# Performance work log

Hardware: AMD Instinct MI355X
Metric: run time of the kernel (lower is better)

## Reference

```python
import jax, jax.numpy as jnp
from jax import lax
import numpy as np

HEADS = 3
DIM_HEAD = 64
INNER = HEADS * DIM_HEAD  # 192
SCALE = DIM_HEAD ** -0.5
BN_EPS = 1e-5


def _sep_conv(x, dw, gamma, beta, mean, var, pw, stride):
    """Depthwise conv (SAME) -> BatchNorm (inference) -> 1x1 pointwise conv."""
    C = x.shape[-1]
    x = lax.conv_general_dilated(
        x, dw, window_strides=(stride, stride), padding='SAME',
        dimension_numbers=('NHWC', 'HWIO', 'NHWC'), feature_group_count=C)
    x = (x - mean) * lax.rsqrt(var + BN_EPS) * gamma + beta
    return jnp.einsum('bhwc,cd->bhwd', x, pw)


def setup_inputs() -> dict:
    key = jax.random.key(0)
    ks = jax.random.split(key, 8)
    B, H, W, C = 8, 56, 56, 192
    return {
        'x': jax.random.normal(ks[0], (B, H, W, C), dtype=jnp.float32),
        'dw_q': jax.random.normal(ks[1], (3, 3, 1, C), dtype=jnp.float32) * 0.1,
        'q_gamma': jnp.ones((C,), jnp.float32),
        'q_beta': jnp.zeros((C,), jnp.float32),
        'q_mean': jnp.zeros((C,), jnp.float32),
        'q_var': jnp.ones((C,), jnp.float32),
        'pw_q': jax.random.normal(ks[2], (C, INNER), dtype=jnp.float32) / np.sqrt(C).astype(np.float32),
        'dw_kv': jax.random.normal(ks[3], (3, 3, 1, C), dtype=jnp.float32) * 0.1,
        'kv_gamma': jnp.ones((C,), jnp.float32),
        'kv_beta': jnp.zeros((C,), jnp.float32),
        'kv_mean': jnp.zeros((C,), jnp.float32),
        'kv_var': jnp.ones((C,), jnp.float32),
        'pw_kv': jax.random.normal(ks[4], (C, 2 * INNER), dtype=jnp.float32) / np.sqrt(C).astype(np.float32),
        'out_w': jax.random.normal(ks[5], (INNER, C), dtype=jnp.float32) / np.sqrt(INNER).astype(np.float32),
        'out_b': jnp.zeros((C,), jnp.float32),
    }


def reference(x, dw_q, q_gamma, q_beta, q_mean, q_var, pw_q,
              dw_kv, kv_gamma, kv_beta, kv_mean, kv_var, pw_kv,
              out_w, out_b):
    B, H, W, C = x.shape
    q = _sep_conv(x, dw_q, q_gamma, q_beta, q_mean, q_var, pw_q, 1)      # [B,H,W,INNER]
    kv = _sep_conv(x, dw_kv, kv_gamma, kv_beta, kv_mean, kv_var, pw_kv, 2)  # [B,H/2,W/2,2*INNER]
    k, v = jnp.split(kv, 2, axis=-1)

    def split_heads(t):
        b, h, w, _ = t.shape
        return t.reshape(b, h * w, HEADS, DIM_HEAD)

    q, k, v = split_heads(q), split_heads(k), split_heads(v)  # [B,N,h,d]
    scores = jnp.einsum('bihd,bjhd->bhij', q, k) * SCALE       # [B,h,Nq,Nkv]
    attn = jax.nn.softmax(scores, axis=-1)
    o = jnp.einsum('bhij,bjhd->bihd', attn, v)                 # [B,Nq,h,d]
    o = o.reshape(B, H, W, INNER)
    return jnp.einsum('bhwc,cd->bhwd', o, out_w) + out_b
```

## Files before the change

### kernel.cpp

```cpp
#include <hip/hip_runtime.h>

namespace {
constexpr int Bb = 8, Hh = 56, Ww = 56, Cc = 192;
constexpr int NQ  = Hh * Ww;
constexpr int NKV = 28 * 28;
constexpr float EPS = 1e-5f;
}

typedef __attribute__((ext_vector_type(8))) short          bf16x8;
typedef __attribute__((ext_vector_type(4))) float          f32x4;
typedef __attribute__((ext_vector_type(8))) unsigned short u16x8;

__device__ inline unsigned short f2b(float f) {
  unsigned u = __builtin_bit_cast(unsigned, f);
  u += 0x7FFFu + ((u >> 16) & 1u);
  return (unsigned short)(u >> 16);
}

__device__ inline uint2 pack4(float a, float b, float c, float d) {
  uint2 r;
  r.x = (unsigned)f2b(a) | ((unsigned)f2b(b) << 16);
  r.y = (unsigned)f2b(c) | ((unsigned)f2b(d) << 16);
  return r;
}

__global__ __launch_bounds__(256) void prep_w_kernel(
    const float* __restrict__ pwq, const float* __restrict__ pwkv,
    const float* __restrict__ outw,
    unsigned short* __restrict__ wq, unsigned short* __restrict__ wkv,
    unsigned short* __restrict__ wo)
{
  int i = blockIdx.x * 256 + threadIdx.x;
  if (i < 36864) {
    int n = i / 192, k = i - n * 192;
    wq[i] = f2b(pwq[k * 192 + n]);
  } else if (i < 110592) {
    int j = i - 36864;
    int n = j / 192, k = j - n * 192;
    wkv[j] = f2b(pwkv[k * 384 + n]);
  } else if (i < 147456) {
    int j = i - 110592;
    int n = j / 192, k = j - n * 192;
    wo[j] = f2b(outw[k * 192 + n]);
  }
}

__global__ __launch_bounds__(256) void dwbn_bf16_kernel(
    const float* __restrict__ x, const float* __restrict__ w,
    const float* __restrict__ gamma, const float* __restrict__ beta,
    const float* __restrict__ mean, const float* __restrict__ var,
    unsigned short* __restrict__ out, int OH, int OW, int stride, int pad)
{
  int idx = blockIdx.x * 256 + threadIdx.x;
  int total = Bb * OH * OW * 48;
  if (idx >= total) return;
  int c4 = idx % 48;
  int t = idx / 48;
  int ow = t % OW; t /= OW;
  int oh = t % OH; int b = t / OH;
  const int c = c4 * 4;

  float4 acc = make_float4(0.f, 0.f, 0.f, 0.f);
#pragma unroll
  for (int kh = 0; kh < 3; ++kh) {
    int ih = oh * stride - pad + kh;
    if (ih < 0 || ih >= Hh) continue;
#pragma unroll
    for (int kw = 0; kw < 3; ++kw) {
      int iw = ow * stride - pad + kw;
      if (iw < 0 || iw >= Ww) continue;
      float4 xv = *(const float4*)&x[((size_t)(b * Hh + ih) * Ww + iw) * Cc + c];
      float4 wv = *(const float4*)&w[(kh * 3 + kw) * Cc + c];
      acc.x += xv.x * wv.x; acc.y += xv.y * wv.y;
      acc.z += xv.z * wv.z; acc.w += xv.w * wv.w;
    }
  }
  float4 gm = *(const float4*)&gamma[c];
  float4 bt = *(const float4*)&beta[c];
  float4 mn = *(const float4*)&mean[c];
  float4 vr = *(const float4*)&var[c];
  float r0 = (acc.x - mn.x) * gm.x / sqrtf(vr.x + EPS) + bt.x;
  float r1 = (acc.y - mn.y) * gm.y / sqrtf(vr.y + EPS) + bt.y;
  float r2 = (acc.z - mn.z) * gm.z / sqrtf(vr.z + EPS) + bt.z;
  float r3 = (acc.w - mn.w) * gm.w / sqrtf(vr.w + EPS) + bt.w;
  const size_t row = (size_t)(b * OH + oh) * OW + ow;
  *reinterpret_cast<uint2*>(&out[row * 192 + c]) = pack4(r0, r1, r2, r3);
}

template <int MODE>
__global__ __launch_bounds__(256) void gemm_mfma(
    const unsigned short* __restrict__ A, const unsigned short* __restrict__ Bt,
    const float* __restrict__ bias, unsigned short* __restrict__ QK,
    unsigned short* __restrict__ Vt, float* __restrict__ O32,
    int N, int NR)
{
  __shared__ unsigned short As[128][72];
  __shared__ unsigned short Bs[64][72];

  const int nbl = N >> 6;
  const int bm = blockIdx.x / nbl, bn = blockIdx.x % nbl;
  const int row0 = bm << 7, col0 = bn << 6;
  const int tid = threadIdx.x;
  const int lane = tid & 63, w = tid >> 6;
  const int lr = lane & 15, lg = lane >> 4;
  const int wm = w >> 1, wn = w & 1;

  f32x4 acc[4][2];
#pragma unroll
  for (int mr = 0; mr < 4; ++mr)
#pragma unroll
    for (int nr = 0; nr < 2; ++nr) acc[mr][nr] = (f32x4){0.f, 0.f, 0.f, 0.f};

  for (int k0 = 0; k0 < 192; k0 += 64) {
    {
      const int r = tid >> 1, c0 = (tid & 1) * 32;
      const unsigned short* src = A + (size_t)(row0 + r) * 192 + k0 + c0;
#pragma unroll
      for (int u = 0; u < 4; ++u)
        *(u16x8*)&As[r][c0 + u * 8] = *(const u16x8*)&src[u * 8];
    }
    {
      const int n = tid >> 2, c0 = (tid & 3) * 16;
      const unsigned short* src = Bt + (size_t)(col0 + n) * 192 + k0 + c0;
#pragma unroll
      for (int u = 0; u < 2; ++u)
        *(u16x8*)&Bs[n][c0 + u * 8] = *(const u16x8*)&src[u * 8];
    }
    __syncthreads();
#pragma unroll
    for (int ks = 0; ks < 2; ++ks) {
      bf16x8 a[4], b[2];
#pragma unroll
      for (int mr = 0; mr < 4; ++mr)
        a[mr] = *(const bf16x8*)&As[wm * 64 + mr * 16 + lr][ks * 32 + lg * 8];
#pragma unroll
      for (int nr = 0; nr < 2; ++nr)
        b[nr] = *(const bf16x8*)&Bs[wn * 32 + nr * 16 + lr][ks * 32 + lg * 8];
#pragma unroll
      for (int mr = 0; mr < 4; ++mr)
#pragma unroll
        for (int nr = 0; nr < 2; ++nr)
          acc[mr][nr] = __builtin_amdgcn_mfma_f32_16x16x32_bf16(a[mr], b[nr], acc[mr][nr], 0, 0, 0);
    }
    __syncthreads();
  }

#pragma unroll
  for (int mr = 0; mr < 4; ++mr) {
#pragma unroll
    for (int nr = 0; nr < 2; ++nr) {
      const int c = col0 + wn * 32 + nr * 16 + lr;
      const int rbase = row0 + wm * 64 + mr * 16 + lg * 4;
      if (MODE == 2) {
        const float bb = bias[c];
#pragma unroll
        for (int j = 0; j < 4; ++j)
          O32[(size_t)(rbase + j) * 192 + c] = acc[mr][nr][j] + bb;
      } else if (MODE == 0 || (MODE == 1 && c < 192)) {
        const int h = c >> 6, d = c & 63;
        const int b = rbase / NR;
        const int n0 = rbase - b * NR;
        const float sc = (MODE == 0) ? 0.125f : 1.0f;
#pragma unroll
        for (int j = 0; j < 4; ++j)
          QK[(((size_t)b * 3 + h) * NR + n0 + j) * 64 + d] = f2b(acc[mr][nr][j] * sc);
      } else {
        const int h = (c - 192) >> 6, d = (c - 192) & 63;
        const int b = rbase / 784;
        const int n0 = rbase - b * 784;
        uint2 v = pack4(acc[mr][nr][0], acc[mr][nr][1], acc[mr][nr][2], acc[mr][nr][3]);
        *reinterpret_cast<uint2*>(&Vt[(((size_t)b * 3 + h) * 64 + d) * 784 + n0]) = v;
      }
    }
  }
}

__global__ __launch_bounds__(256) void attn_mfma_kernel(
    const unsigned short* __restrict__ Qb, const unsigned short* __restrict__ Kb,
    const unsigned short* __restrict__ Vtb, unsigned short* __restrict__ Ob)
{
  __shared__ unsigned short Ks[64][72];
  __shared__ unsigned short Vts[64][72];
  __shared__ unsigned short Ps[64][66];
  __shared__ float ls[4][16];

  const int blk = blockIdx.x;
  const int qt = blk % 49;
  const int bh = blk / 49;
  const int n0 = qt * 64;
  const int tid = threadIdx.x;
  const int lane = tid & 63;
  const int w = tid >> 6;
  const int lr = lane & 15, lg = lane >> 4;
  const int row = tid >> 2, cc = tid & 3;

  const unsigned short* qrow = Qb + ((size_t)bh * NQ + n0 + w * 16 + lr) * 64;
  const bf16x8 aq0 = *(const bf16x8*)&qrow[lg * 8];
  const bf16x8 aq1 = *(const bf16x8*)&qrow[32 + lg * 8];

  const unsigned short* kbase = Kb + (size_t)bh * NKV * 64;
  const unsigned short* vrow  = Vtb + ((size_t)bh * 64 + row) * NKV;

  f32x4 oacc[4];
#pragma unroll
  for (int db = 0; db < 4; ++db) oacc[db] = (f32x4){0.f, 0.f, 0.f, 0.f};
  float lsum = 0.f;

  for (int kt = 0; kt < 13; ++kt) {
    __syncthreads();
    {
      const int kvg = (kt * 64 + row < NKV) ? kt * 64 + row : NKV - 1;
      const unsigned short* kp = kbase + (size_t)kvg * 64;
      *(u16x8*)&Ks[row][cc * 8]      = *(const u16x8*)&kp[cc * 8];
      *(u16x8*)&Ks[row][cc * 8 + 32] = *(const u16x8*)&kp[cc * 8 + 32];
#pragma unroll
      for (int u = 0; u < 2; ++u) {
        const int c8 = cc + 4 * u;
        const int kv0 = kt * 64 + c8 * 8;
        u16x8 vv = {0, 0, 0, 0, 0, 0, 0, 0};
        if (kv0 < NKV) vv = *(const u16x8*)&vrow[kv0];
        *(u16x8*)&Vts[row][c8 * 8] = vv;
      }
    }
    __syncthreads();

    f32x4 st[4];
#pragma unroll
    for (int nb = 0; nb < 4; ++nb) {
      const bf16x8 bk0 = *(const bf16x8*)&Ks[nb * 16 + lr][lg * 8];
      const bf16x8 bk1 = *(const bf16x8*)&Ks[nb * 16 + lr][32 + lg * 8];
      f32x4 a = (f32x4){0.f, 0.f, 0.f, 0.f};
      a = __builtin_amdgcn_mfma_f32_16x16x32_bf16(bk0, aq0, a, 0, 0, 0);
      a = __builtin_amdgcn_mfma_f32_16x16x32_bf16(bk1, aq1, a, 0, 0, 0);
      st[nb] = a;
    }

    const int kvb = kt * 64 + lg * 4;
#pragma unroll
    for (int nb = 0; nb < 4; ++nb) {
      float p[4];
#pragma unroll
      for (int r = 0; r < 4; ++r)
        p[r] = (kvb + nb * 16 + r < NKV) ? __expf(st[nb][r]) : 0.f;
      lsum += (p[0] + p[1]) + (p[2] + p[3]);
      uint2 u = pack4(p[0], p[1], p[2], p[3]);
      *reinterpret_cast<uint2*>(&Ps[w * 16 + lr][nb * 16 + lg * 4]) = u;
    }

    const bf16x8 pa0 = *(const bf16x8*)&Ps[w * 16 + lr][lg * 8];
    const bf16x8 pa1 = *(const bf16x8*)&Ps[w * 16 + lr][32 + lg * 8];
#pragma unroll
    for (int db = 0; db < 4; ++db) {
      const bf16x8 vb0 = *(const bf16x8*)&Vts[db * 16 + lr][lg * 8];
      const bf16x8 vb1 = *(const bf16x8*)&Vts[db * 16 + lr][32 + lg * 8];
      oacc[db] = __builtin_amdgcn_mfma_f32_16x16x32_bf16(pa0, vb0, oacc[db], 0, 0, 0);
      oacc[db] = __builtin_amdgcn_mfma_f32_16x16x32_bf16(pa1, vb1, oacc[db], 0, 0, 0);
    }
  }

  float l = lsum;
  l += __shfl_xor(l, 16);
  l += __shfl_xor(l, 32);
  if (lg == 0) ls[w][lr] = l;
  const float4 lv = *(const float4*)&ls[w][lg * 4];

  const int b = bh / 3, h = bh - b * 3;
  float linv[4];
#pragma unroll
  for (int j = 0; j < 4; ++j) linv[j] = 1.f / ((&lv.x)[j]);
#pragma unroll
  for (int j = 0; j < 4; ++j) {
    const int qg = n0 + w * 16 + lg * 4 + j;
    unsigned short* orow = Ob + ((size_t)b * NQ + qg) * 192 + h * 64 + lr;
#pragma unroll
    for (int db = 0; db < 4; ++db) orow[db * 16] = f2b(oacc[db][j] * linv[j]);
  }
}

extern "C" void kernel_launch(void* const* d_in, const int* in_sizes, int n_in,
                              void* d_out, int out_size, void* d_ws, size_t ws_size,
                              hipStream_t stream)
{
  const float* x        = (const float*)d_in[0];
  const float* dw_q     = (const float*)d_in[1];
  const float* q_gamma  = (const float*)d_in[2];
  const float* q_beta   = (const float*)d_in[3];
  const float* q_mean   = (const float*)d_in[4];
  const float* q_var    = (const float*)d_in[5];
  const float* pw_q     = (const float*)d_in[6];
  const float* dw_kv    = (const float*)d_in[7];
  const float* kv_gamma = (const float*)d_in[8];
  const float* kv_beta  = (const float*)d_in[9];
  const float* kv_mean  = (const float*)d_in[10];
  const float* kv_var   = (const float*)d_in[11];
  const float* pw_kv    = (const float*)d_in[12];
  const float* out_w    = (const float*)d_in[13];
  const float* out_b    = (const float*)d_in[14];
  float* out = (float*)d_out;

  unsigned short* dwbuf = (unsigned short*)d_ws;
  unsigned short* Qbuf  = dwbuf + (size_t)25088 * 192;
  unsigned short* Kbuf  = Qbuf + (size_t)24 * 3136 * 64;
  unsigned short* Vtbuf = Kbuf + (size_t)24 * 784 * 64;
  unsigned short* Wq    = Vtbuf + (size_t)24 * 784 * 64;
  unsigned short* Wkv   = Wq + 36864;
  unsigned short* Wo    = Wkv + 73728;

  prep_w_kernel<<<576, 256, 0, stream>>>(pw_q, pw_kv, out_w, Wq, Wkv, Wo);
  dwbn_bf16_kernel<<<(25088 * 48 + 255) / 256, 256, 0, stream>>>(
      x, dw_q, q_gamma, q_beta, q_mean, q_var, dwbuf, 56, 56, 1, 1);
  gemm_mfma<0><<<196 * 3, 256, 0, stream>>>(dwbuf, Wq, nullptr, Qbuf, nullptr, nullptr, 192, 3136);
  dwbn_bf16_kernel<<<(6272 * 48 + 255) / 256, 256, 0, stream>>>(
      x, dw_kv, kv_gamma, kv_beta, kv_mean, kv_var, dwbuf, 28, 28, 2, 0);
  gemm_mfma<1><<<49 * 6, 256, 0, stream>>>(dwbuf, Wkv, nullptr, Kbuf, Vtbuf, nullptr, 384, 784);
  attn_mfma_kernel<<<8 * 3 * 49, 256, 0, stream>>>(Qbuf, Kbuf, Vtbuf, dwbuf);
  gemm_mfma<2><<<196 * 3, 256, 0, stream>>>(dwbuf, Wo, out_b, nullptr, nullptr, out, 192, 25088);
}
```

Measured before the change: 109.4 us.

## Merge prep kernels, fuse QKV GEMMs, prefetch K/V tiles in attention with exp2

Merges the weight transpose and both depthwise+BN passes into one launch, and runs the Q and KV projections as a single GEMM launch. This cuts the pipeline from seven kernels to four. The attention loop now holds the next K/V tile in registers while computing on the current one. The Q scale is folded with log2(e) so the kernel can use exp2f. The per-element tail mask is replaced by a separate 16-row tail step that zero-pads the P tile. It also changes bf16 rounding to the library conversion and widens the Ps padding, which raises register pressure and adds tail logic that must stay correct.

```diff
diff --git a/kernel.cpp b/kernel.cpp
--- a/kernel.cpp
+++ b/kernel.cpp
@@ -1,10 +1,12 @@
 #include <hip/hip_runtime.h>
+#include <hip/hip_bf16.h>
 
 namespace {
 constexpr int Bb = 8, Hh = 56, Ww = 56, Cc = 192;
 constexpr int NQ  = Hh * Ww;
 constexpr int NKV = 28 * 28;
 constexpr float EPS = 1e-5f;
+constexpr float QSCALE = 0.125f * 1.4426950408889634f;
 }
 
 typedef __attribute__((ext_vector_type(8))) short          bf16x8;
@@ -12,9 +14,8 @@
 typedef __attribute__((ext_vector_type(8))) unsigned short u16x8;
 
 __device__ inline unsigned short f2b(float f) {
-  unsigned u = __builtin_bit_cast(unsigned, f);
-  u += 0x7FFFu + ((u >> 16) & 1u);
-  return (unsigned short)(u >> 16);
+  __hip_bfloat16 h = __float2bfloat16(f);
+  return __builtin_bit_cast(unsigned short, h);
 }
 
 __device__ inline uint2 pack4(float a, float b, float c, float d) {
@@ -24,36 +25,12 @@
   return r;
 }
 
-__global__ __launch_bounds__(256) void prep_w_kernel(
-    const float* __restrict__ pwq, const float* __restrict__ pwkv,
-    const float* __restrict__ outw,
-    unsigned short* __restrict__ wq, unsigned short* __restrict__ wkv,
-    unsigned short* __restrict__ wo)
-{
-  int i = blockIdx.x * 256 + threadIdx.x;
-  if (i < 36864) {
-    int n = i / 192, k = i - n * 192;
-    wq[i] = f2b(pwq[k * 192 + n]);
-  } else if (i < 110592) {
-    int j = i - 36864;
-    int n = j / 192, k = j - n * 192;
-    wkv[j] = f2b(pwkv[k * 384 + n]);
-  } else if (i < 147456) {
-    int j = i - 110592;
-    int n = j / 192, k = j - n * 192;
-    wo[j] = f2b(outw[k * 192 + n]);
-  }
-}
-
-__global__ __launch_bounds__(256) void dwbn_bf16_kernel(
-    const float* __restrict__ x, const float* __restrict__ w,
+__device__ inline void dwbn_body(
+    int idx, const float* __restrict__ x, const float* __restrict__ w,
     const float* __restrict__ gamma, const float* __restrict__ beta,
     const float* __restrict__ mean, const float* __restrict__ var,
     unsigned short* __restrict__ out, int OH, int OW, int stride, int pad)
 {
-  int idx = blockIdx.x * 256 + threadIdx.x;
-  int total = Bb * OH * OW * 48;
-  if (idx >= total) return;
   int c4 = idx % 48;
   int t = idx / 48;
   int ow = t % OW; t /= OW;
@@ -87,18 +64,62 @@
   *reinterpret_cast<uint2*>(&out[row * 192 + c]) = pack4(r0, r1, r2, r3);
 }
 
-template <int MODE>
-__global__ __launch_bounds__(256) void gemm_mfma(
-    const unsigned short* __restrict__ A, const unsigned short* __restrict__ Bt,
-    const float* __restrict__ bias, unsigned short* __restrict__ QK,
-    unsigned short* __restrict__ Vt, float* __restrict__ O32,
-    int N, int NR)
+__global__ __launch_bounds__(256) void stage1_kernel(
+    const float* __restrict__ x,
+    const float* __restrict__ dw_q, const float* __restrict__ q_gamma,
+    const float* __restrict__ q_beta, const float* __restrict__ q_mean,
+    const float* __restrict__ q_var,
+    const float* __restrict__ dw_kv, const float* __restrict__ kv_gamma,
+    const float* __restrict__ kv_beta, const float* __restrict__ kv_mean,
+    const float* __restrict__ kv_var,
+    const float* __restrict__ pwq, const float* __restrict__ pwkv,
+    const float* __restrict__ outw,
+    unsigned short* __restrict__ dwq, unsigned short* __restrict__ dwkv,
+    unsigned short* __restrict__ wq, unsigned short* __restrict__ wkv,
+    unsigned short* __restrict__ wo)
+{
+  const int blk = blockIdx.x;
+  if (blk < 4704) {
+    dwbn_body(blk * 256 + threadIdx.x, x, dw_q, q_gamma, q_beta, q_mean, q_var,
+              dwq, 56, 56, 1, 1);
+  } else if (blk < 5880) {
+    dwbn_body((blk - 4704) * 256 + threadIdx.x, x, dw_kv, kv_gamma, kv_beta,
+              kv_mean, kv_var, dwkv, 28, 28, 2, 0);
+  } else {
+    int i = (blk - 5880) * 256 + threadIdx.x;
+    if (i < 36864) {
+      int n = i / 192, k = i - n * 192;
+      wq[i] = f2b(pwq[k * 192 + n]);
+    } else if (i < 110592) {
+      int j = i - 36864;
+      int n = j / 192, k = j - n * 192;
+      wkv[j] = f2b(pwkv[k * 384 + n]);
+    } else {
+      int j = i - 110592;
+      int n = j / 192, k = j - n * 192;
+      wo[j] = f2b(outw[k * 192 + n]);
+    }
+  }
+}
+
+__global__ __launch_bounds__(256) void gemm_qkv_kernel(
+    const unsigned short* __restrict__ dwq, const unsigned short* __restrict__ dwkv,
+    const unsigned short* __restrict__ Wq, const unsigned short* __restrict__ Wkv,
+    unsigned short* __restrict__ Qbuf, unsigned short* __restrict__ Kbuf,
+    unsigned short* __restrict__ Vtbuf)
 {
   __shared__ unsigned short As[128][72];
   __shared__ unsigned short Bs[64][72];
 
-  const int nbl = N >> 6;
-  const int bm = blockIdx.x / nbl, bn = blockIdx.x % nbl;
+  const int blk = blockIdx.x;
+  const bool isQ = blk < 588;
+  const int lb = isQ ? blk : blk - 588;
+  const unsigned short* __restrict__ A  = isQ ? dwq : dwkv;
+  const unsigned short* __restrict__ Bt = isQ ? Wq : Wkv;
+  const int nbl = isQ ? 3 : 6;
+  const int NR  = isQ ? 3136 : 784;
+
+  const int bm = lb / nbl, bn = lb % nbl;
   const int row0 = bm << 7, col0 = bn << 6;
   const int tid = threadIdx.x;
   const int lane = tid & 63, w = tid >> 6;
@@ -151,26 +172,95 @@
     for (int nr = 0; nr < 2; ++nr) {
       const int c = col0 + wn * 32 + nr * 16 + lr;
       const int rbase = row0 + wm * 64 + mr * 16 + lg * 4;
-      if (MODE == 2) {
-        const float bb = bias[c];
+      if (isQ) {
+        const int h = c >> 6, d = c & 63;
+        const int b = rbase / 3136;
+        const int n0 = rbase - b * 3136;
 #pragma unroll
         for (int j = 0; j < 4; ++j)
-          O32[(size_t)(rbase + j) * 192 + c] = acc[mr][nr][j] + bb;
-      } else if (MODE == 0 || (MODE == 1 && c < 192)) {
+          Qbuf[(((size_t)b * 3 + h) * 3136 + n0 + j) * 64 + d] = f2b(acc[mr][nr][j] * QSCALE);
+      } else if (c < 192) {
         const int h = c >> 6, d = c & 63;
-        const int b = rbase / NR;
-        const int n0 = rbase - b * NR;
-        const float sc = (MODE == 0) ? 0.125f : 1.0f;
+        const int b = rbase / 784;
+        const int n0 = rbase - b * 784;
 #pragma unroll
         for (int j = 0; j < 4; ++j)
-          QK[(((size_t)b * 3 + h) * NR + n0 + j) * 64 + d] = f2b(acc[mr][nr][j] * sc);
+          Kbuf[(((size_t)b * 3 + h) * 784 + n0 + j) * 64 + d] = f2b(acc[mr][nr][j]);
       } else {
         const int h = (c - 192) >> 6, d = (c - 192) & 63;
         const int b = rbase / 784;
         const int n0 = rbase - b * 784;
         uint2 v = pack4(acc[mr][nr][0], acc[mr][nr][1], acc[mr][nr][2], acc[mr][nr][3]);
-        *reinterpret_cast<uint2*>(&Vt[(((size_t)b * 3 + h) * 64 + d) * 784 + n0]) = v;
+        *reinterpret_cast<uint2*>(&Vtbuf[(((size_t)b * 3 + h) * 64 + d) * 784 + n0]) = v;
       }
+    }
+  }
+}
+
+__global__ __launch_bounds__(256) void gemm_out_kernel(
+    const unsigned short* __restrict__ A, const unsigned short* __restrict__ Bt,
+    const float* __restrict__ bias, float* __restrict__ O32)
+{
+  __shared__ unsigned short As[128][72];
+  __shared__ unsigned short Bs[64][72];
+
+  const int bm = blockIdx.x / 3, bn = blockIdx.x % 3;
+  const int row0 = bm << 7, col0 = bn << 6;
+  const int tid = threadIdx.x;
+  const int lane = tid & 63, w = tid >> 6;
+  const int lr = lane & 15, lg = lane >> 4;
+  const int wm = w >> 1, wn = w & 1;
+
+  f32x4 acc[4][2];
+#pragma unroll
+  for (int mr = 0; mr < 4; ++mr)
+#pragma unroll
+    for (int nr = 0; nr < 2; ++nr) acc[mr][nr] = (f32x4){0.f, 0.f, 0.f, 0.f};
+
+  for (int k0 = 0; k0 < 192; k0 += 64) {
+    {
+      const int r = tid >> 1, c0 = (tid & 1) * 32;
+      const unsigned short* src = A + (size_t)(row0 + r) * 192 + k0 + c0;
+#pragma unroll
+      for (int u = 0; u < 4; ++u)
+        *(u16x8*)&As[r][c0 + u * 8] = *(const u16x8*)&src[u * 8];
+    }
+    {
+      const int n = tid >> 2, c0 = (tid & 3) * 16;
+      const unsigned short* src = Bt + (size_t)(col0 + n) * 192 + k0 + c0;
+#pragma unroll
+      for (int u = 0; u < 2; ++u)
+        *(u16x8*)&Bs[n][c0 + u * 8] = *(const u16x8*)&src[u * 8];
+    }
+    __syncthreads();
+#pragma unroll
+    for (int ks = 0; ks < 2; ++ks) {
+      bf16x8 a[4], b[2];
+#pragma unroll
+      for (int mr = 0; mr < 4; ++mr)
+        a[mr] = *(const bf16x8*)&As[wm * 64 + mr * 16 + lr][ks * 32 + lg * 8];
+#pragma unroll
+      for (int nr = 0; nr < 2; ++nr)
+        b[nr] = *(const bf16x8*)&Bs[wn * 32 + nr * 16 + lr][ks * 32 + lg * 8];
+#pragma unroll
+      for (int mr = 0; mr < 4; ++mr)
+#pragma unroll
+        for (int nr = 0; nr < 2; ++nr)
+          acc[mr][nr] = __builtin_amdgcn_mfma_f32_16x16x32_bf16(a[mr], b[nr], acc[mr][nr], 0, 0, 0);
+    }
+    __syncthreads();
+  }
+
+#pragma unroll
+  for (int mr = 0; mr < 4; ++mr) {
+#pragma unroll
+    for (int nr = 0; nr < 2; ++nr) {
+      const int c = col0 + wn * 32 + nr * 16 + lr;
+      const int rbase = row0 + wm * 64 + mr * 16 + lg * 4;
+      const float bb = bias[c];
+#pragma unroll
+      for (int j = 0; j < 4; ++j)
+        O32[(size_t)(rbase + j) * 192 + c] = acc[mr][nr][j] + bb;
     }
   }
 }
@@ -181,7 +271,7 @@
 {
   __shared__ unsigned short Ks[64][72];
   __shared__ unsigned short Vts[64][72];
-  __shared__ unsigned short Ps[64][66];
+  __shared__ unsigned short Ps[64][72];
   __shared__ float ls[4][16];
 
   const int blk = blockIdx.x;
@@ -192,37 +282,48 @@
   const int lane = tid & 63;
   const int w = tid >> 6;
   const int lr = lane & 15, lg = lane >> 4;
-  const int row = tid >> 2, cc = tid & 3;
+  const int srow = w * 16 + lr;
+  const int scc  = lg;
 
   const unsigned short* qrow = Qb + ((size_t)bh * NQ + n0 + w * 16 + lr) * 64;
   const bf16x8 aq0 = *(const bf16x8*)&qrow[lg * 8];
   const bf16x8 aq1 = *(const bf16x8*)&qrow[32 + lg * 8];
 
   const unsigned short* kbase = Kb + (size_t)bh * NKV * 64;
-  const unsigned short* vrow  = Vtb + ((size_t)bh * 64 + row) * NKV;
+  const unsigned short* vrow  = Vtb + ((size_t)bh * 64 + srow) * NKV;
+
+  u16x8 kr0, kr1, vr0, vr1;
+  {
+    const unsigned short* kp = kbase + (size_t)srow * 64;
+    kr0 = *(const u16x8*)&kp[scc * 8];
+    kr1 = *(const u16x8*)&kp[scc * 8 + 32];
+    vr0 = *(const u16x8*)&vrow[scc * 8];
+    vr1 = *(const u16x8*)&vrow[scc * 8 + 32];
+  }
+  *(u16x8*)&Ks[srow][scc * 8]       = kr0;
+  *(u16x8*)&Ks[srow][scc * 8 + 32]  = kr1;
+  *(u16x8*)&Vts[srow][scc * 8]      = vr0;
+  *(u16x8*)&Vts[srow][scc * 8 + 32] = vr1;
+  __syncthreads();
 
   f32x4 oacc[4];
 #pragma unroll
   for (int db = 0; db < 4; ++db) oacc[db] = (f32x4){0.f, 0.f, 0.f, 0.f};
   float lsum = 0.f;
 
-  for (int kt = 0; kt < 13; ++kt) {
-    __syncthreads();
+  for (int kt = 0; kt < 12; ++kt) {
     {
-      const int kvg = (kt * 64 + row < NKV) ? kt * 64 + row : NKV - 1;
+      const int nk = kt + 1;
+      const int kvg = (nk * 64 + srow < NKV) ? nk * 64 + srow : NKV - 1;
       const unsigned short* kp = kbase + (size_t)kvg * 64;
-      *(u16x8*)&Ks[row][cc * 8]      = *(const u16x8*)&kp[cc * 8];
-      *(u16x8*)&Ks[row][cc * 8 + 32] = *(const u16x8*)&kp[cc * 8 + 32];
-#pragma unroll
-      for (int u = 0; u < 2; ++u) {
-        const int c8 = cc + 4 * u;
-        const int kv0 = kt * 64 + c8 * 8;
-        u16x8 vv = {0, 0, 0, 0, 0, 0, 0, 0};
-        if (kv0 < NKV) vv = *(const u16x8*)&vrow[kv0];
-        *(u16x8*)&Vts[row][c8 * 8] = vv;
-      }
-    }
-    __syncthreads();
+      kr0 = *(const u16x8*)&kp[scc * 8];
+      kr1 = *(const u16x8*)&kp[scc * 8 + 32];
+      const int vb = nk * 64 + scc * 8;
+      const int vc0 = (vb      <= NKV - 8) ? vb      : NKV - 8;
+      const int vc1 = (vb + 32 <= NKV - 8) ? vb + 32 : NKV - 8;
+      vr0 = *(const u16x8*)&vrow[vc0];
+      vr1 = *(const u16x8*)&vrow[vc1];
+    }
 
     f32x4 st[4];
 #pragma unroll
@@ -235,13 +336,11 @@
       st[nb] = a;
     }
 
-    const int kvb = kt * 64 + lg * 4;
 #pragma unroll
     for (int nb = 0; nb < 4; ++nb) {
       float p[4];
 #pragma unroll
-      for (int r = 0; r < 4; ++r)
-        p[r] = (kvb + nb * 16 + r < NKV) ? __expf(st[nb][r]) : 0.f;
+      for (int r = 0; r < 4; ++r) p[r] = exp2f(st[nb][r]);
       lsum += (p[0] + p[1]) + (p[2] + p[3]);
       uint2 u = pack4(p[0], p[1], p[2], p[3]);
       *reinterpret_cast<uint2*>(&Ps[w * 16 + lr][nb * 16 + lg * 4]) = u;
@@ -255,6 +354,34 @@
       const bf16x8 vb1 = *(const bf16x8*)&Vts[db * 16 + lr][32 + lg * 8];
       oacc[db] = __builtin_amdgcn_mfma_f32_16x16x32_bf16(pa0, vb0, oacc[db], 0, 0, 0);
       oacc[db] = __builtin_amdgcn_mfma_f32_16x16x32_bf16(pa1, vb1, oacc[db], 0, 0, 0);
+    }
+
+    __syncthreads();
+    *(u16x8*)&Ks[srow][scc * 8]       = kr0;
+    *(u16x8*)&Ks[srow][scc * 8 + 32]  = kr1;
+    *(u16x8*)&Vts[srow][scc * 8]      = vr0;
+    *(u16x8*)&Vts[srow][scc * 8 + 32] = vr1;
+    __syncthreads();
+  }
+
+  {
+    const bf16x8 bk0 = *(const bf16x8*)&Ks[lr][lg * 8];
+    const bf16x8 bk1 = *(const bf16x8*)&Ks[lr][32 + lg * 8];
+    f32x4 a = (f32x4){0.f, 0.f, 0.f, 0.f};
+    a = __builtin_amdgcn_mfma_f32_16x16x32_bf16(bk0, aq0, a, 0, 0, 0);
+    a = __builtin_amdgcn_mfma_f32_16x16x32_bf16(bk1, aq1, a, 0, 0, 0);
+    float p[4];
+#pragma unroll
+    for (int r = 0; r < 4; ++r) p[r] = exp2f(a[r]);
+    lsum += (p[0] + p[1]) + (p[2] + p[3]);
+    *reinterpret_cast<uint2*>(&Ps[w * 16 + lr][lg * 4]) = pack4(p[0], p[1], p[2], p[3]);
+    uint2 z; z.x = 0u; z.y = 0u;
+    *reinterpret_cast<uint2*>(&Ps[w * 16 + lr][16 + lg * 4]) = z;
+    const bf16x8 pa0 = *(const bf16x8*)&Ps[w * 16 + lr][lg * 8];
+#pragma unroll
+    for (int db = 0; db < 4; ++db) {
+      const bf16x8 vb0 = *(const bf16x8*)&Vts[db * 16 + lr][lg * 8];
+      oacc[db] = __builtin_amdgcn_mfma_f32_16x16x32_bf16(pa0, vb0, oacc[db], 0, 0, 0);
     }
   }
 
@@ -298,21 +425,20 @@
   const float* out_b    = (const float*)d_in[14];
   float* out = (float*)d_out;
 
-  unsigned short* dwbuf = (unsigned short*)d_ws;
-  unsigned short* Qbuf  = dwbuf + (size_t)25088 * 192;
-  unsigned short* Kbuf  = Qbuf + (size_t)24 * 3136 * 64;
-  unsigned short* Vtbuf = Kbuf + (size_t)24 * 784 * 64;
+  unsigned short* dwq   = (unsigned short*)d_ws;
+  unsigned short* dwkv  = dwq   + (size_t)25088 * 192;
+  unsigned short* Qbuf  = dwkv  + (size_t)6272 * 192;
+  unsigned short* Kbuf  = Qbuf  + (size_t)24 * 3136 * 64;
+  unsigned short* Vtbuf = Kbuf  + (size_t)24 * 784 * 64;
   unsigned short* Wq    = Vtbuf + (size_t)24 * 784 * 64;
   unsigned short* Wkv   = Wq + 36864;
   unsigned short* Wo    = Wkv + 73728;
 
-  prep_w_kernel<<<576, 256, 0, stream>>>(pw_q, pw_kv, out_w, Wq, Wkv, Wo);
-  dwbn_bf16_kernel<<<(25088 * 48 + 255) / 256, 256, 0, stream>>>(
-      x, dw_q, q_gamma, q_beta, q_mean, q_var, dwbuf, 56, 56, 1, 1);
-  gemm_mfma<0><<<196 * 3, 256, 0, stream>>>(dwbuf, Wq, nullptr, Qbuf, nullptr, nullptr, 192, 3136);
-  dwbn_bf16_kernel<<<(6272 * 48 + 255) / 256, 256, 0, stream>>>(
-      x, dw_kv, kv_gamma, kv_beta, kv_mean, kv_var, dwbuf, 28, 28, 2, 0);
-  gemm_mfma<1><<<49 * 6, 256, 0, stream>>>(dwbuf, Wkv, nullptr, Kbuf, Vtbuf, nullptr, 384, 784);
-  attn_mfma_kernel<<<8 * 3 * 49, 256, 0, stream>>>(Qbuf, Kbuf, Vtbuf, dwbuf);
-  gemm_mfma<2><<<196 * 3, 256, 0, stream>>>(dwbuf, Wo, out_b, nullptr, nullptr, out, 192, 25088);
-}
+  stage1_kernel<<<6456, 256, 0, stream>>>(
+      x, dw_q, q_gamma, q_beta, q_mean, q_var,
+      dw_kv, kv_gamma, kv_beta, kv_mean, kv_var,
+      pw_q, pw_kv, out_w, dwq, dwkv, Wq, Wkv, Wo);
+  gemm_qkv_kernel<<<882, 256, 0, stream>>>(dwq, dwkv, Wq, Wkv, Qbuf, Kbuf, Vtbuf);
+  attn_mfma_kernel<<<8 * 3 * 49, 256, 0, stream>>>(Qbuf, Kbuf, Vtbuf, dwq);
+  gemm_out_kernel<<<588, 256, 0, stream>>>(dwq, Wo, out_b, out);
+}
```

After: 89.00 us. 18.6% less time.
